# Kernel tuning notes

Hardware: AMD Instinct MI355X
Metric: run time of the kernel (lower is better)

Reference implementation:

```python
import jax, jax.numpy as jnp
import numpy as np

N, P, T, D = 25000, 100000, 4, 128
DIN = 4 * D + 4  # 516
LEAKY = 0.001


def setup_inputs() -> dict:
    key = jax.random.key(0)
    ks = jax.random.split(key, 12)
    inp = {
        "coords": jax.random.normal(ks[0], (N, T, 3), jnp.float32),
        "propers": jax.random.randint(ks[1], (P, 4), 0, N, jnp.int64),
        "encoded": jax.random.normal(ks[2], (N, D), jnp.float32),
        "t": jax.random.uniform(ks[3], (T,), jnp.float32),
        "answer": jax.random.normal(ks[4], (N, T, 3), jnp.float32),
        # AggregateMLP(516 -> 128 -> 128 -> 128 -> 2), LeakyReLU(0.001) between
        "W0": jax.random.normal(ks[5], (DIN, D), jnp.float32) / np.sqrt(DIN),
        "b0": jnp.zeros((D,), jnp.float32),
        "W1": jax.random.normal(ks[6], (D, D), jnp.float32) / np.sqrt(D),
        "b1": jnp.zeros((D,), jnp.float32),
        "W2": jax.random.normal(ks[7], (D, D), jnp.float32) / np.sqrt(D),
        "b2": jnp.zeros((D,), jnp.float32),
        "W3": jax.random.normal(ks[8], (D, 2), jnp.float32) / np.sqrt(D),
        "b3": jnp.zeros((2,), jnp.float32),
    }
    return inp


def _forward(coords, propers, encoded, t, answer, W0, b0, W1, b1, W2, b2, W3, b3):
    p0, p1, p2, p3 = propers[:, 0], propers[:, 1], propers[:, 2], propers[:, 3]
    c0, c1, c2, c3 = coords[p0], coords[p1], coords[p2], coords[p3]  # [P,T,3]
    u1 = c1 - c0
    u2 = c2 - c1
    u3 = c3 - c2
    u1xu2 = jnp.cross(u1, u2, axis=-1)
    u2xu3 = jnp.cross(u2, u3, axis=-1)
    u2_norm = jnp.linalg.norm(u2, axis=-1, keepdims=True)
    u1yu2 = u1 * u2_norm
    theta = jnp.arctan2((u1yu2 * u2xu3).sum(-1), (u1xu2 * u2xu3).sum(-1))  # [P,T]
    dr = c0 - c3  # [P,T,3]
    dl = jnp.sqrt(jnp.clip(jnp.square(dr).sum(-1), 1e-12))  # [P,T]
    dh = dr / dl[..., None]

    Pn, Tn = propers.shape[0], t.shape[0]
    bcast = lambda e: jnp.broadcast_to(e[:, None, :], (Pn, Tn, e.shape[-1]))
    feats = jnp.concatenate(
        [
            bcast(encoded[p0]),
            bcast(encoded[p1]),
            bcast(encoded[p2]),
            bcast(encoded[p3]),
            jnp.broadcast_to(t.reshape(1, Tn, 1), (Pn, Tn, 1)),
            jnp.sin(theta)[..., None],
            jnp.cos(theta)[..., None],
            dl[..., None],
        ],
        axis=2,
    )  # [P,T,516]

    h = jax.nn.leaky_relu(feats @ W0 + b0, LEAKY)
    h = jax.nn.leaky_relu(h @ W1 + b1, LEAKY)
    h = jax.nn.leaky_relu(h @ W2 + b2, LEAKY)
    delta = h @ W3 + b3  # [P,T,2]

    out = answer.at[p0].add(-0.5 * delta[:, :, 0:1] * dh)
    out = out.at[p3].add(0.5 * delta[:, :, 1:2] * dh)
    return out


def reference(coords, propers, encoded, t, answer, W0, b0, W1, b1, W2, b2, W3, b3):
    return _forward(coords, propers, encoded, t, answer, W0, b0, W1, b1, W2, b2, W3, b3)
```

## Files before the change

kernel.cpp:

```cpp
#include <hip/hip_runtime.h>
#include <hip/hip_bf16.h>

#define NN 25000
#define PP 100000
#define TT 4
#define DD 128
#define LEAKY 0.001f

#define PB 32
#define ROWS 128

typedef __bf16 bf16;
typedef __bf16 bf16x8 __attribute__((ext_vector_type(8)));
typedef float  f32x4  __attribute__((ext_vector_type(4)));

#define OFF_W0SW  0u
#define OFF_W1SW  131072u
#define OFF_W2SW  163840u
#define OFF_W3SW  196608u
#define OFF_WTB   200704u
#define OFF_W5B   201728u
#define OFF_E     202496u
#define WS_END    25802496u

#define PR_W0SW  65536
#define PR_W1SW  16384
#define PR_W2SW  16384
#define PR_W3SW  2048
#define PR_WTB   512
#define PR_W5B   384
#define PR_COPY4 75000
#define PR_TOTAL (PR_W0SW + PR_W1SW + PR_W2SW + PR_W3SW + PR_WTB + PR_W5B + PR_COPY4)

#define LGKM0() asm volatile("s_waitcnt lgkmcnt(0)" ::: "memory")

__device__ __forceinline__ void gload_lds16(const void* g, void* l) {
    __builtin_amdgcn_global_load_lds(
        (const __attribute__((address_space(1))) void*)g,
        (__attribute__((address_space(3))) void*)l, 16, 0, 0);
}

__global__ __launch_bounds__(256) void prep_kernel(
    const float* __restrict__ W0, const float* __restrict__ W1,
    const float* __restrict__ W2, const float* __restrict__ W3,
    const float* __restrict__ answer, const float* __restrict__ tvec,
    const float* __restrict__ b0,
    bf16* __restrict__ W0sw, bf16* __restrict__ W1sw, bf16* __restrict__ W2sw,
    bf16* __restrict__ W3sw, bf16* __restrict__ WtB, bf16* __restrict__ W5B,
    float* __restrict__ out)
{
    int idx = blockIdx.x * 256 + threadIdx.x;
    if (idx < PR_W0SW) {
        int j = idx & 7, lane = (idx >> 3) & 63, c = idx >> 9;
        int fr = lane & 15, quad = lane >> 4;
        int kc = c & 15, iwv = c >> 4;
        int k = kc * 32 + quad * 8 + j;
        W0sw[idx] = (bf16)W0[k * 128 + iwv * 16 + fr];
        return;
    }
    idx -= PR_W0SW;
    if (idx < PR_W1SW) {
        int j = idx & 7, lane = (idx >> 3) & 63, c = idx >> 9;
        int fr = lane & 15, quad = lane >> 4;
        int kc = c & 3, nt = c >> 2;
        int k = kc * 32 + quad * 8 + j;
        W1sw[idx] = (bf16)W1[k * 128 + nt * 16 + fr];
        return;
    }
    idx -= PR_W1SW;
    if (idx < PR_W2SW) {
        int j = idx & 7, lane = (idx >> 3) & 63, c = idx >> 9;
        int fr = lane & 15, quad = lane >> 4;
        int kc = c & 3, nt = c >> 2;
        int k = kc * 32 + quad * 8 + j;
        W2sw[idx] = (bf16)W2[k * 128 + nt * 16 + fr];
        return;
    }
    idx -= PR_W2SW;
    if (idx < PR_W3SW) {
        int j = idx & 7, lane = (idx >> 3) & 63, kc = idx >> 9;
        int fr = lane & 15, quad = lane >> 4;
        int k = kc * 32 + quad * 8 + j;
        W3sw[idx] = (fr < 2) ? (bf16)W3[k * 2 + fr] : (bf16)0.0f;
        return;
    }
    idx -= PR_W3SW;
    if (idx < PR_WTB) {
        int t = idx >> 7, j = idx & 127;
        WtB[idx] = (bf16)(tvec[t] * W0[512 * 128 + j] + b0[j]);
        return;
    }
    idx -= PR_WTB;
    if (idx < PR_W5B) {
        W5B[idx] = (bf16)W0[(513 + (idx >> 7)) * 128 + (idx & 127)];
        return;
    }
    idx -= PR_W5B;
    if (idx < PR_COPY4) { ((float4*)out)[idx] = ((const float4*)answer)[idx]; }
}

__global__ __launch_bounds__(512) void prep_e_kernel(
    const float* __restrict__ encoded, const bf16* __restrict__ W0sw,
    bf16* __restrict__ E)
{
    __shared__ bf16 sA[128][136];
    __shared__ bf16 sT[128][40];
    const int tid = threadIdx.x;
    const int row0 = (blockIdx.x >> 2) * 128;
    const int ntb  = blockIdx.x & 3;
    for (int c = tid; c < 4096; c += 512) {
        int row = c >> 5, seg = c & 31;
        int rr = row0 + row; if (rr >= NN) rr = NN - 1;
        float4 v = *(const float4*)(encoded + (size_t)rr * 128 + seg * 4);
        bf16 pk[4] = {(bf16)v.x, (bf16)v.y, (bf16)v.z, (bf16)v.w};
        *(uint2*)(&sA[row][seg * 4]) = *(const uint2*)pk;
    }
    __syncthreads();
    const int wv = tid >> 6, lane = tid & 63;
    const int fr = lane & 15, quad = lane >> 4;
    const bf16* aBase = &sA[wv * 16 + fr][quad * 8];
    bf16x8 aFv[4];
    #pragma unroll
    for (int kcc = 0; kcc < 4; ++kcc) aFv[kcc] = *(const bf16x8*)(aBase + kcc * 32);
    const int orow = tid >> 2, oseg = tid & 3;
    #pragma unroll
    for (int i = 0; i < 4; ++i) {
        #pragma unroll
        for (int ntl = 0; ntl < 2; ++ntl) {
            int nt = ntb * 2 + ntl;
            f32x4 acc = {0.f, 0.f, 0.f, 0.f};
            #pragma unroll
            for (int kcc = 0; kcc < 4; ++kcc) {
                bf16x8 bF = *(const bf16x8*)(W0sw + ((size_t)nt * 16 + i * 4 + kcc) * 512 + lane * 8);
                acc = __builtin_amdgcn_mfma_f32_16x16x32_bf16(aFv[kcc], bF, acc, 0, 0, 0);
            }
            #pragma unroll
            for (int reg = 0; reg < 4; ++reg)
                sT[wv * 16 + quad * 4 + reg][ntl * 16 + fr] = (bf16)acc[reg];
        }
        LGKM0();
        bf16x8 ev = *(const bf16x8*)(&sT[orow][oseg * 8]);
        LGKM0();
        if (row0 + orow < NN)
            *(bf16x8*)(E + ((size_t)i * NN + row0 + orow) * 128 + ntb * 32 + oseg * 8) = ev;
    }
}

__global__ __launch_bounds__(512, 4) void main_kernel(
    const float* __restrict__ coords, const int* __restrict__ propers,
    const float* __restrict__ b1, const float* __restrict__ b2,
    const float* __restrict__ b3,
    const bf16* __restrict__ E, const bf16* __restrict__ W1sw,
    const bf16* __restrict__ W2sw, const bf16* __restrict__ W3sw,
    const bf16* __restrict__ WtB, const bf16* __restrict__ W5B,
    float* __restrict__ out)
{
    __shared__ __align__(16) bf16 sH[8][16][136];
    __shared__ __align__(16) bf16 sW[18432];
    __shared__ float sScr[8][16][6];
    __shared__ int   sNd[8][8];

    const int tid  = threadIdx.x;
    const int wv   = tid >> 6, lane = tid & 63;
    const int fr   = lane & 15, quad = lane >> 4;
    const int pw   = blockIdx.x * PB + wv * 4;

    {
        const char* g1 = (const char*)W1sw;
        char* l = (char*)&sW[0];
        #pragma unroll
        for (int r2 = 0; r2 < 4; ++r2)
            gload_lds16(g1 + r2 * 8192 + wv * 1024 + lane * 16,
                        l + r2 * 8192 + wv * 1024);
        if (wv < 4)
            gload_lds16((const char*)W3sw + wv * 1024 + lane * 16,
                        l + 32768 + wv * 1024);
    }

    int4 pv = *(const int4*)(propers + (size_t)(pw + quad) * 4);
    bf16x8 e0 = *(const bf16x8*)(E + ((size_t)0 * NN + pv.x) * 128 + fr * 8);
    bf16x8 e1 = *(const bf16x8*)(E + ((size_t)1 * NN + pv.y) * 128 + fr * 8);
    bf16x8 e2 = *(const bf16x8*)(E + ((size_t)2 * NN + pv.z) * 128 + fr * 8);
    bf16x8 e3 = *(const bf16x8*)(E + ((size_t)3 * NN + pv.w) * 128 + fr * 8);
    if (fr == 0) { sNd[wv][quad * 2] = pv.x; sNd[wv][quad * 2 + 1] = pv.w; }
    bf16x8 w3v = *(const bf16x8*)(W5B + 0 * 128 + fr * 8);
    bf16x8 w4v = *(const bf16x8*)(W5B + 1 * 128 + fr * 8);
    bf16x8 w5v = *(const bf16x8*)(W5B + 2 * 128 + fr * 8);

    float b1r[8], b2r[8];
    #pragma unroll
    for (int i = 0; i < 8; ++i) {
        b1r[i] = b1[i * 16 + fr];
        b2r[i] = b2[i * 16 + fr];
    }
    float b3r = (fr < 2) ? b3[fr] : 0.0f;

    float snl = 0.f, csl = 1.f, dll = 0.f;
    if (lane < 16) {
        int pp_ = lane >> 2, t = lane & 3;
        int4 pg = *(const int4*)(propers + (size_t)(pw + pp_) * 4);
        const float* c0 = coords + (size_t)pg.x * 12 + t * 3;
        const float* c1 = coords + (size_t)pg.y * 12 + t * 3;
        const float* c2 = coords + (size_t)pg.z * 12 + t * 3;
        const float* c3 = coords + (size_t)pg.w * 12 + t * 3;
        float u1x = c1[0]-c0[0], u1y = c1[1]-c0[1], u1z = c1[2]-c0[2];
        float u2x = c2[0]-c1[0], u2y = c2[1]-c1[1], u2z = c2[2]-c1[2];
        float u3x = c3[0]-c2[0], u3y = c3[1]-c2[1], u3z = c3[2]-c2[2];
        float ax = u1y*u2z - u1z*u2y, ay = u1z*u2x - u1x*u2z, az = u1x*u2y - u1y*u2x;
        float bx = u2y*u3z - u2z*u3y, by = u2z*u3x - u2x*u3z, bz = u2x*u3y - u2y*u3x;
        float u2n = sqrtf(u2x*u2x + u2y*u2y + u2z*u2z);
        float num = u2n * (u1x*bx + u1y*by + u1z*bz);
        float den = ax*bx + ay*by + az*bz;
        float hyp = sqrtf(num*num + den*den);
        if (hyp > 1e-30f) { float ih = 1.0f / hyp; snl = num * ih; csl = den * ih; }
        else { snl = 0.0f; csl = 1.0f; }
        float drx = c0[0]-c3[0], dry = c0[1]-c3[1], drz = c0[2]-c3[2];
        dll = sqrtf(fmaxf(drx*drx + dry*dry + drz*drz, 1e-12f));
        float il = 1.0f / dll;
        sScr[wv][lane][0] = drx * il;
        sScr[wv][lane][1] = dry * il;
        sScr[wv][lane][2] = drz * il;
    }

    {
        float g[8], w3f[8], w4f[8], w5f[8];
        #pragma unroll
        for (int j = 0; j < 8; ++j) {
            g[j]   = (float)e0[j] + (float)e1[j] + (float)e2[j] + (float)e3[j];
            w3f[j] = (float)w3v[j]; w4f[j] = (float)w4v[j]; w5f[j] = (float)w5v[j];
        }
        #pragma unroll
        for (int t = 0; t < 4; ++t) {
            int r = quad * 4 + t;
            bf16x8 wtv = *(const bf16x8*)(WtB + t * 128 + fr * 8);
            float sn = __shfl(snl, r), cs = __shfl(csl, r), dl = __shfl(dll, r);
            bf16 hv[8];
            #pragma unroll
            for (int j = 0; j < 8; ++j) {
                float v = g[j] + (float)wtv[j] + sn * w3f[j] + cs * w4f[j] + dl * w5f[j];
                v = fmaxf(v, LEAKY * v);
                hv[j] = (bf16)v;
            }
            *(bf16x8*)(&sH[wv][r][fr * 8]) = *(const bf16x8*)hv;
        }
    }
    __syncthreads();

#define DENSE_LAYER(BR)                                                         \
    {                                                                           \
        LGKM0();            \
        bf16x8 aF[4];                                                           \
        const bf16* aRow = &sH[wv][fr][quad * 8];                               \
        _Pragma("unroll")                                                       \
        for (int kc = 0; kc < 4; ++kc)                                          \
            aF[kc] = *(const bf16x8*)(aRow + kc * 32);                          \
        LGKM0();      \
        _Pragma("unroll")                                                       \
        for (int hh = 0; hh < 2; ++hh) {                                        \
            f32x4 acc[4];                                                       \
            _Pragma("unroll")                                                   \
            for (int nt = 0; nt < 4; ++nt) acc[nt] = (f32x4){0.f,0.f,0.f,0.f};  \
            _Pragma("unroll")                                                   \
            for (int kc = 0; kc < 4; ++kc) {                                    \
                _Pragma("unroll")                                               \
                for (int nt = 0; nt < 4; ++nt) {                                \
                    bf16x8 bF = *(const bf16x8*)(sW +                           \
                        ((hh * 4 + nt) * 4 + kc) * 512 + lane * 8);             \
                    acc[nt] = __builtin_amdgcn_mfma_f32_16x16x32_bf16(          \
                        aF[kc], bF, acc[nt], 0, 0, 0);                          \
                }                                                               \
            }                                                                   \
            _Pragma("unroll")                                                   \
            for (int nt = 0; nt < 4; ++nt) {                                    \
                int j = (hh * 4 + nt) * 16 + fr;                                \
                float bb = BR[hh * 4 + nt];                                     \
                _Pragma("unroll")                                               \
                for (int reg = 0; reg < 4; ++reg) {                             \
                    float v = acc[nt][reg] + bb;                                \
                    v = fmaxf(v, LEAKY * v);                                    \
                    sH[wv][quad * 4 + reg][j] = (bf16)v;                        \
                }                                                               \
            }                                                                   \
        }                                                                       \
    }

    DENSE_LAYER(b1r)
    __syncthreads();
    {
        const char* g2 = (const char*)W2sw;
        char* l = (char*)&sW[0];
        #pragma unroll
        for (int r2 = 0; r2 < 4; ++r2)
            gload_lds16(g2 + r2 * 8192 + wv * 1024 + lane * 16,
                        l + r2 * 8192 + wv * 1024);
    }
    __syncthreads();
    DENSE_LAYER(b2r)

    {
        LGKM0();
        bf16x8 aF[4];
        const bf16* aRow = &sH[wv][fr][quad * 8];
        #pragma unroll
        for (int kc = 0; kc < 4; ++kc)
            aF[kc] = *(const bf16x8*)(aRow + kc * 32);
        f32x4 dacc = {0.f, 0.f, 0.f, 0.f};
        #pragma unroll
        for (int kc = 0; kc < 4; ++kc) {
            bf16x8 bF = *(const bf16x8*)(sW + 16384 + kc * 512 + lane * 8);
            dacc = __builtin_amdgcn_mfma_f32_16x16x32_bf16(aF[kc], bF, dacc, 0, 0, 0);
        }
        if (fr < 2) {
            #pragma unroll
            for (int reg = 0; reg < 4; ++reg)
                sScr[wv][quad * 4 + reg][3 + fr] = dacc[reg] + b3r;
        }
    }

    LGKM0();
    for (int idx = lane; idx < 96; idx += 64) {
        int r = idx / 6, c = idx - (idx / 6) * 6;
        int side = c / 3, ax = c - side * 3;
        int node = sNd[wv][(r >> 2) * 2 + side];
        float dval = (side ? 0.5f : -0.5f) * sScr[wv][r][3 + side];
        atomicAdd(out + (size_t)node * 12 + (r & 3) * 3 + ax, dval * sScr[wv][r][ax]);
    }
#undef DENSE_LAYER
}

extern "C" void kernel_launch(void* const* d_in, const int* in_sizes, int n_in,
                              void* d_out, int out_size, void* d_ws, size_t ws_size,
                              hipStream_t stream) {
    const float* coords  = (const float*)d_in[0];
    const int*   propers = (const int*)d_in[1];
    const float* encoded = (const float*)d_in[2];
    const float* tvec    = (const float*)d_in[3];
    const float* answer  = (const float*)d_in[4];
    const float* W0 = (const float*)d_in[5];
    const float* b0 = (const float*)d_in[6];
    const float* W1 = (const float*)d_in[7];
    const float* b1 = (const float*)d_in[8];
    const float* W2 = (const float*)d_in[9];
    const float* b2 = (const float*)d_in[10];
    const float* W3 = (const float*)d_in[11];
    const float* b3 = (const float*)d_in[12];
    float* out = (float*)d_out;
    char* ws = (char*)d_ws;
    bf16* W0sw = (bf16*)(ws + OFF_W0SW);
    bf16* W1sw = (bf16*)(ws + OFF_W1SW);
    bf16* W2sw = (bf16*)(ws + OFF_W2SW);
    bf16* W3sw = (bf16*)(ws + OFF_W3SW);
    bf16* WtB  = (bf16*)(ws + OFF_WTB);
    bf16* W5B  = (bf16*)(ws + OFF_W5B);
    bf16* E    = (bf16*)(ws + OFF_E);

    int prep_blocks = (PR_TOTAL + 255) / 256;
    prep_kernel<<<prep_blocks, 256, 0, stream>>>(W0, W1, W2, W3, answer, tvec, b0,
                                                 W0sw, W1sw, W2sw, W3sw, WtB, W5B, out);
    prep_e_kernel<<<196 * 4, 512, 0, stream>>>(encoded, W0sw, E);
    main_kernel<<<PP / PB, 512, 0, stream>>>(coords, propers, b1, b2, b3,
                                             E, W1sw, W2sw, W3sw, WtB, W5B, out);
}
```

Before: 169.7 us.

## Vectorize weight swizzle stores and halve prep_e block size for more blocks

The weight-prep kernel now has each thread produce eight bf16 values and write them as one 16-byte store, instead of one scalar bf16 store per thread. This cuts the prep thread count by eight. The encoded-projection prep kernel switches from 128-row, 512-thread blocks to 64-row, 256-thread blocks, roughly doubling the grid to spread work across more CUs. The intent is to shorten the small prep kernels that run before the main kernel. The unseen body of prep_e must still index correctly with the halved tile and thread count.

```diff
diff --git a/kernel.cpp b/kernel.cpp
--- a/kernel.cpp
+++ b/kernel.cpp
@@ -23,12 +23,12 @@
 #define OFF_E     202496u
 #define WS_END    25802496u
 
-#define PR_W0SW  65536
-#define PR_W1SW  16384
-#define PR_W2SW  16384
-#define PR_W3SW  2048
-#define PR_WTB   512
-#define PR_W5B   384
+#define PR_W0SW  8192
+#define PR_W1SW  2048
+#define PR_W2SW  2048
+#define PR_W3SW  256
+#define PR_WTB   64
+#define PR_W5B   48
 #define PR_COPY4 75000
 #define PR_TOTAL (PR_W0SW + PR_W1SW + PR_W2SW + PR_W3SW + PR_WTB + PR_W5B + PR_COPY4)
 
@@ -51,64 +51,86 @@
 {
     int idx = blockIdx.x * 256 + threadIdx.x;
     if (idx < PR_W0SW) {
-        int j = idx & 7, lane = (idx >> 3) & 63, c = idx >> 9;
+        int lane = idx & 63, c = idx >> 6;
         int fr = lane & 15, quad = lane >> 4;
         int kc = c & 15, iwv = c >> 4;
-        int k = kc * 32 + quad * 8 + j;
-        W0sw[idx] = (bf16)W0[k * 128 + iwv * 16 + fr];
+        bf16 v[8];
+        #pragma unroll
+        for (int j = 0; j < 8; ++j)
+            v[j] = (bf16)W0[(kc * 32 + quad * 8 + j) * 128 + iwv * 16 + fr];
+        *(bf16x8*)(W0sw + c * 512 + lane * 8) = *(const bf16x8*)v;
         return;
     }
     idx -= PR_W0SW;
     if (idx < PR_W1SW) {
-        int j = idx & 7, lane = (idx >> 3) & 63, c = idx >> 9;
+        int lane = idx & 63, c = idx >> 6;
         int fr = lane & 15, quad = lane >> 4;
         int kc = c & 3, nt = c >> 2;
-        int k = kc * 32 + quad * 8 + j;
-        W1sw[idx] = (bf16)W1[k * 128 + nt * 16 + fr];
+        bf16 v[8];
+        #pragma unroll
+        for (int j = 0; j < 8; ++j)
+            v[j] = (bf16)W1[(kc * 32 + quad * 8 + j) * 128 + nt * 16 + fr];
+        *(bf16x8*)(W1sw + c * 512 + lane * 8) = *(const bf16x8*)v;
         return;
     }
     idx -= PR_W1SW;
     if (idx < PR_W2SW) {
-        int j = idx & 7, lane = (idx >> 3) & 63, c = idx >> 9;
+        int lane = idx & 63, c = idx >> 6;
         int fr = lane & 15, quad = lane >> 4;
         int kc = c & 3, nt = c >> 2;
-        int k = kc * 32 + quad * 8 + j;
-        W2sw[idx] = (bf16)W2[k * 128 + nt * 16 + fr];
+        bf16 v[8];
+        #pragma unroll
+        for (int j = 0; j < 8; ++j)
+            v[j] = (bf16)W2[(kc * 32 + quad * 8 + j) * 128 + nt * 16 + fr];
+        *(bf16x8*)(W2sw + c * 512 + lane * 8) = *(const bf16x8*)v;
         return;
     }
     idx -= PR_W2SW;
     if (idx < PR_W3SW) {
-        int j = idx & 7, lane = (idx >> 3) & 63, kc = idx >> 9;
+        int lane = idx & 63, kc = idx >> 6;
         int fr = lane & 15, quad = lane >> 4;
-        int k = kc * 32 + quad * 8 + j;
-        W3sw[idx] = (fr < 2) ? (bf16)W3[k * 2 + fr] : (bf16)0.0f;
+        bf16 v[8];
+        #pragma unroll
+        for (int j = 0; j < 8; ++j)
+            v[j] = (fr < 2) ? (bf16)W3[(kc * 32 + quad * 8 + j) * 2 + fr] : (bf16)0.0f;
+        *(bf16x8*)(W3sw + kc * 512 + lane * 8) = *(const bf16x8*)v;
         return;
     }
     idx -= PR_W3SW;
     if (idx < PR_WTB) {
-        int t = idx >> 7, j = idx & 127;
-        WtB[idx] = (bf16)(tvec[t] * W0[512 * 128 + j] + b0[j]);
+        int t = idx >> 4, s = idx & 15;
+        float tv = tvec[t];
+        bf16 v[8];
+        #pragma unroll
+        for (int j = 0; j < 8; ++j)
+            v[j] = (bf16)(tv * W0[512 * 128 + s * 8 + j] + b0[s * 8 + j]);
+        *(bf16x8*)(WtB + t * 128 + s * 8) = *(const bf16x8*)v;
         return;
     }
     idx -= PR_WTB;
     if (idx < PR_W5B) {
-        W5B[idx] = (bf16)W0[(513 + (idx >> 7)) * 128 + (idx & 127)];
+        int r = idx >> 4, s = idx & 15;
+        bf16 v[8];
+        #pragma unroll
+        for (int j = 0; j < 8; ++j)
+            v[j] = (bf16)W0[(513 + r) * 128 + s * 8 + j];
+        *(bf16x8*)(W5B + r * 128 + s * 8) = *(const bf16x8*)v;
         return;
     }
     idx -= PR_W5B;
     if (idx < PR_COPY4) { ((float4*)out)[idx] = ((const float4*)answer)[idx]; }
 }
 
-__global__ __launch_bounds__(512) void prep_e_kernel(
+__global__ __launch_bounds__(256) void prep_e_kernel(
     const float* __restrict__ encoded, const bf16* __restrict__ W0sw,
     bf16* __restrict__ E)
 {
-    __shared__ bf16 sA[128][136];
-    __shared__ bf16 sT[128][40];
+    __shared__ bf16 sA[64][136];
+    __shared__ bf16 sT[64][40];
     const int tid = threadIdx.x;
-    const int row0 = (blockIdx.x >> 2) * 128;
+    const int row0 = (blockIdx.x >> 2) * 64;
     const int ntb  = blockIdx.x & 3;
-    for (int c = tid; c < 4096; c += 512) {
+    for (int c = tid; c < 2048; c += 256) {
         int row = c >> 5, seg = c & 31;
         int rr = row0 + row; if (rr >= NN) rr = NN - 1;
         float4 v = *(const float4*)(encoded + (size_t)rr * 128 + seg * 4);
@@ -357,7 +379,7 @@
     int prep_blocks = (PR_TOTAL + 255) / 256;
     prep_kernel<<<prep_blocks, 256, 0, stream>>>(W0, W1, W2, W3, answer, tvec, b0,
                                                  W0sw, W1sw, W2sw, W3sw, WtB, W5B, out);
-    prep_e_kernel<<<196 * 4, 512, 0, stream>>>(encoded, W0sw, E);
+    prep_e_kernel<<<391 * 4, 256, 0, stream>>>(encoded, W0sw, E);
     main_kernel<<<PP / PB, 512, 0, stream>>>(coords, propers, b1, b2, b3,
                                              E, W1sw, W2sw, W3sw, WtB, W5B, out);
 }
```

Measured after the change: 167.0 us. Within noise of the previous version (-1.6%).
